# Kernel optimization log

Measured on AMD Instinct MI355X. Metric: run time of the kernel, lower is better.

Reference implementation:

```python
import jax, jax.numpy as jnp
import numpy as np

D = 1024
H = 16
HD = D // H
FF = 4 * D


def layer_norm(x, gamma, beta, eps=1e-5):
    mu = jnp.mean(x, axis=-1, keepdims=True)
    var = jnp.var(x, axis=-1, keepdims=True)
    return (x - mu) * jax.lax.rsqrt(var + eps) * gamma + beta


def setup_inputs() -> dict:
    key = jax.random.key(0)
    ks = jax.random.split(key, 12)
    B, Nq, Nkv = 8, 512, 1024
    s = 0.02
    return {
        "query": jax.random.normal(ks[0], (B, Nq, D), jnp.float32),
        "key_value": jax.random.normal(ks[1], (B, Nkv, D), jnp.float32),
        "key_padding_mask": jax.random.randint(ks[2], (B, Nkv), 0, 2) > 0,
        "nq_gamma": jnp.ones((D,), jnp.float32),
        "nq_beta": jnp.zeros((D,), jnp.float32),
        "nkv_gamma": jnp.ones((D,), jnp.float32),
        "nkv_beta": jnp.zeros((D,), jnp.float32),
        "in_proj_w": jax.random.normal(ks[3], (3 * D, D), jnp.float32) * s,
        "in_proj_b": jnp.zeros((3 * D,), jnp.float32),
        "out_w": jax.random.normal(ks[4], (D, D), jnp.float32) * s,
        "out_b": jnp.zeros((D,), jnp.float32),
        "nff_gamma": jnp.ones((D,), jnp.float32),
        "nff_beta": jnp.zeros((D,), jnp.float32),
        "ff1_w": jax.random.normal(ks[5], (FF, D), jnp.float32) * s,
        "ff1_b": jnp.zeros((FF,), jnp.float32),
        "ff2_w": jax.random.normal(ks[6], (D, FF), jnp.float32) * s,
        "ff2_b": jnp.zeros((D,), jnp.float32),
    }


def reference(query, key_value, key_padding_mask, nq_gamma, nq_beta, nkv_gamma,
              nkv_beta, in_proj_w, in_proj_b, out_w, out_b, nff_gamma, nff_beta,
              ff1_w, ff1_b, ff2_w, ff2_b):
    B, Nq, _ = query.shape
    Nkv = key_value.shape[1]

    q_in = layer_norm(query, nq_gamma, nq_beta)
    kv_in = layer_norm(key_value, nkv_gamma, nkv_beta)

    # packed in-projection as in torch MultiheadAttention
    wq, wk, wv = in_proj_w[:D], in_proj_w[D:2 * D], in_proj_w[2 * D:]
    bq, bk, bv = in_proj_b[:D], in_proj_b[D:2 * D], in_proj_b[2 * D:]
    q = (q_in @ wq.T + bq).reshape(B, Nq, H, HD).transpose(0, 2, 1, 3)   # b h q d
    k = (kv_in @ wk.T + bk).reshape(B, Nkv, H, HD).transpose(0, 2, 1, 3)  # b h k d
    v = (kv_in @ wv.T + bv).reshape(B, Nkv, H, HD).transpose(0, 2, 1, 3)

    scale = 1.0 / np.sqrt(HD).astype(np.float32)
    scores = jnp.einsum('bhqd,bhkd->bhqk', q, k) * scale
    neg = jnp.finfo(scores.dtype).min
    scores = jnp.where(key_padding_mask[:, None, None, :], neg, scores)
    attn = jax.nn.softmax(scores, axis=-1)                  # (B,H,Nq,Nkv)
    ctx = jnp.einsum('bhqk,bhkd->bhqd', attn, v)
    ctx = ctx.transpose(0, 2, 1, 3).reshape(B, Nq, D)
    attended = ctx @ out_w.T + out_b
    attn_weights = jnp.mean(attn, axis=1)                   # averaged over heads

    x = query + attended
    h = layer_norm(x, nff_gamma, nff_beta)
    h = jax.nn.gelu(h @ ff1_w.T + ff1_b, approximate=False)
    x = x + (h @ ff2_w.T + ff2_b)
    return (x, attn_weights)
```

## Files before the change

kernel.cpp:

```cpp
#include <hip/hip_runtime.h>
#include <hip/hip_bf16.h>
#include <math.h>

#define D    1024
#define NQ   512
#define NKV  1024
#define BATCH 8
#define NH   16
#define HD   64
#define FFD  4096

typedef short bf16x8 __attribute__((ext_vector_type(8)));
typedef float f32x4  __attribute__((ext_vector_type(4)));

static __device__ __forceinline__ float bf2f(__hip_bfloat16 x){ return __bfloat162float(x); }
static __device__ __forceinline__ unsigned short f2bbits(float f){
    __hip_bfloat16 h = __float2bfloat16(f);
    return *(unsigned short*)&h;
}

static __device__ __forceinline__ void gload_lds16(const __hip_bfloat16* g, __hip_bfloat16* l){
    __builtin_amdgcn_global_load_lds(
        (const __attribute__((address_space(1))) void*)g,
        (__attribute__((address_space(3))) void*)l,
        16, 0, 0);
}

__global__ __launch_bounds__(256) void cvt_w_kernel(const float* __restrict__ in,
                                                    __hip_bfloat16* __restrict__ out, int n)
{
    int i = blockIdx.x*256 + threadIdx.x;
    if (i < n) out[i] = __float2bfloat16(in[i]);
}

__global__ __launch_bounds__(256) void ln_kernel(
    const float* __restrict__ x, const float* __restrict__ gamma, const float* __restrict__ beta,
    __hip_bfloat16* __restrict__ out)
{
    int row = blockIdx.x, t = threadIdx.x;
    __shared__ float wsum[4];
    __shared__ float stat[2];
    float4 v = *(const float4*)&x[(size_t)row*D + t*4];
    float s = v.x+v.y+v.z+v.w;
    #pragma unroll
    for (int o=32;o>0;o>>=1) s += __shfl_down(s, o);
    if ((t&63)==0) wsum[t>>6] = s;
    __syncthreads();
    if (t==0) stat[0] = (wsum[0]+wsum[1]+wsum[2]+wsum[3])*(1.f/D);
    __syncthreads();
    float mu = stat[0];
    float d0=v.x-mu, d1=v.y-mu, d2=v.z-mu, d3=v.w-mu;
    float s2 = d0*d0+d1*d1+d2*d2+d3*d3;
    #pragma unroll
    for (int o=32;o>0;o>>=1) s2 += __shfl_down(s2, o);
    if ((t&63)==0) wsum[t>>6] = s2;
    __syncthreads();
    if (t==0) stat[1] = rsqrtf((wsum[0]+wsum[1]+wsum[2]+wsum[3])*(1.f/D) + 1e-5f);
    __syncthreads();
    float rs = stat[1];
    const float4 g = *(const float4*)&gamma[t*4];
    const float4 b = *(const float4*)&beta[t*4];
    union { unsigned short u[4]; short4 s4; } pk;
    pk.u[0]=f2bbits(d0*rs*g.x+b.x); pk.u[1]=f2bbits(d1*rs*g.y+b.y);
    pk.u[2]=f2bbits(d2*rs*g.z+b.z); pk.u[3]=f2bbits(d3*rs*g.w+b.w);
    *(short4*)&out[(size_t)row*D + t*4] = pk.s4;
}

#define BM 128
#define BN 128
#define BK 32

static __device__ __forceinline__ void stage128(
    const __hip_bfloat16* __restrict__ A, const __hip_bfloat16* __restrict__ W,
    int K, int bm, int bn, int k0,
    __hip_bfloat16* as, __hip_bfloat16* bs, int w, int srow, int scol)
{
    #pragma unroll
    for (int rep=0; rep<2; rep++){
        int ti = (w<<1) + rep;
        gload_lds16(&A[(size_t)(bm + ti*16 + srow)*K + k0 + scol], &as[ti*16*BK]);
        gload_lds16(&W[(size_t)(bn + ti*16 + srow)*K + k0 + scol], &bs[ti*16*BK]);
    }
}

static __device__ __forceinline__ void compute128(
    const __hip_bfloat16* as, const __hip_bfloat16* bs,
    int wm, int wn, int quad, int l16, f32x4 acc[4][4])
{
    bf16x8 af[4], bfr[4];
    #pragma unroll
    for (int i=0;i<4;i++) af[i]  = *(const bf16x8*)&as[(wm + 16*i + l16)*BK + quad*8];
    #pragma unroll
    for (int j=0;j<4;j++) bfr[j] = *(const bf16x8*)&bs[(wn + 16*j + l16)*BK + quad*8];
    #pragma unroll
    for (int i=0;i<4;i++)
        #pragma unroll
        for (int j=0;j<4;j++)
            acc[i][j] = __builtin_amdgcn_mfma_f32_16x16x32_bf16(af[i], bfr[j], acc[i][j], 0, 0, 0);
}

static __device__ __forceinline__ void gemm_loop(
    const __hip_bfloat16* __restrict__ A, const __hip_bfloat16* __restrict__ W,
    int K, int bm, int bn,
    __hip_bfloat16* As0, __hip_bfloat16* Bs0, __hip_bfloat16* As1, __hip_bfloat16* Bs1,
    f32x4 acc[4][4])
{
    const int t = threadIdx.x;
    const int w = t >> 6, lane = t & 63;
    const int quad = lane >> 4, l16 = lane & 15;
    const int wm = (w >> 1) * 64, wn = (w & 1) * 64;
    const int srow = lane >> 2, scol = (lane & 3) << 3;

    stage128(A, W, K, bm, bn, 0, As0, Bs0, w, srow, scol);
    __syncthreads();
    const int nt = K >> 5;
    for (int ts = 0; ts < nt; ts += 2){
        stage128(A, W, K, bm, bn, (ts+1)<<5, As1, Bs1, w, srow, scol);
        compute128(As0, Bs0, wm, wn, quad, l16, acc);
        __syncthreads();
        if (ts + 2 < nt)
            stage128(A, W, K, bm, bn, (ts+2)<<5, As0, Bs0, w, srow, scol);
        compute128(As1, Bs1, wm, wn, quad, l16, acc);
        __syncthreads();
    }
}

__global__ __launch_bounds__(256) void gemm_mfma_kernel(
    const __hip_bfloat16* __restrict__ A, const __hip_bfloat16* __restrict__ Wb,
    const float* __restrict__ bias, int biasOff,
    const float* __restrict__ residIn, const float* __restrict__ residF,
    float* __restrict__ Cf, __hip_bfloat16* __restrict__ Cb,
    int M, int N, int K, int gelu)
{
    __shared__ __hip_bfloat16 As0[BM*BK], Bs0[BN*BK], As1[BM*BK], Bs1[BN*BK];
    int bm = blockIdx.y * BM, bn = blockIdx.x * BN;
    f32x4 acc[4][4];
    #pragma unroll
    for (int i=0;i<4;i++)
        #pragma unroll
        for (int j=0;j<4;j++) acc[i][j] = (f32x4){0.f,0.f,0.f,0.f};

    gemm_loop(A, Wb, K, bm, bn, As0, Bs0, As1, Bs1, acc);

    const int t = threadIdx.x;
    const int w = t >> 6, lane = t & 63;
    const int quad = lane >> 4, l16 = lane & 15;
    const int wm = (w >> 1) * 64, wn = (w & 1) * 64;
    #pragma unroll
    for (int i=0;i<4;i++){
        #pragma unroll
        for (int j=0;j<4;j++){
            int colg = bn + wn + 16*j + l16;
            float bv = bias[biasOff + colg];
            #pragma unroll
            for (int r=0;r<4;r++){
                int rowg = bm + wm + 16*i + quad*4 + r;
                float vv = acc[i][j][r] + bv;
                if (gelu) vv = 0.5f*vv*(1.f + erff(vv*0.70710678118654752f));
                size_t idx = (size_t)rowg*N + colg;
                if (residIn) vv += residIn[idx];
                if (residF)  vv += residF[idx];
                if (Cf) Cf[idx] = vv;
                if (Cb) Cb[idx] = __float2bfloat16(vv);
            }
        }
    }
}

__global__ __launch_bounds__(256) void qkv_kernel(
    const __hip_bfloat16* __restrict__ qln, const __hip_bfloat16* __restrict__ kvln,
    const __hip_bfloat16* __restrict__ wip, const float* __restrict__ ipb,
    __hip_bfloat16* __restrict__ qb, __hip_bfloat16* __restrict__ kb,
    __hip_bfloat16* __restrict__ vbT)
{
    __shared__ __hip_bfloat16 As0[BM*BK], Bs0[BN*BK], As1[BM*BK], Bs1[BN*BK];
    int id = blockIdx.x;
    const __hip_bfloat16 *A, *W;
    int bm, bn, isq;
    if (id < 1024){ isq = 0; A = kvln; W = wip + (size_t)D*D; bn = (id & 15)*BN; bm = (id >> 4)*BM; }
    else { int qid = id - 1024; isq = 1; A = qln; W = wip; bn = (qid & 7)*BN; bm = (qid >> 3)*BM; }

    f32x4 acc[4][4];
    #pragma unroll
    for (int i=0;i<4;i++)
        #pragma unroll
        for (int j=0;j<4;j++) acc[i][j] = (f32x4){0.f,0.f,0.f,0.f};

    gemm_loop(A, W, 1024, bm, bn, As0, Bs0, As1, Bs1, acc);

    const int t = threadIdx.x;
    const int w = t >> 6, lane = t & 63;
    const int quad = lane >> 4, l16 = lane & 15;
    const int wm = (w >> 1) * 64, wn = (w & 1) * 64;
    #pragma unroll
    for (int i=0;i<4;i++){
        #pragma unroll
        for (int j=0;j<4;j++){
            int colg = bn + wn + 16*j + l16;
            float bv = ipb[(isq ? 0 : D) + colg];
            if (isq){
                #pragma unroll
                for (int r=0;r<4;r++){
                    int rowg = bm + wm + 16*i + quad*4 + r;
                    qb[(size_t)rowg*D + colg] = __float2bfloat16(acc[i][j][r] + bv);
                }
            } else if (colg < 1024){
                #pragma unroll
                for (int r=0;r<4;r++){
                    int rowg = bm + wm + 16*i + quad*4 + r;
                    kb[(size_t)rowg*D + colg] = __float2bfloat16(acc[i][j][r] + bv);
                }
            } else {
                union { unsigned short u[4]; short4 s4; } pk;
                #pragma unroll
                for (int r=0;r<4;r++) pk.u[r] = f2bbits(acc[i][j][r] + bv);
                int rowg0 = bm + wm + 16*i + quad*4;
                int bb = rowg0 >> 10, kvi = rowg0 & 1023;
                int c = colg - 1024, hh = c >> 6, dd = c & 63;
                *(short4*)&vbT[(((size_t)bb*NH + hh)*HD + dd)*NKV + kvi] = pk.s4;
            }
        }
    }
}

#define QT 16
#define PLD (NKV + 8)
__global__ __launch_bounds__(512) void attn_kernel(
    const __hip_bfloat16* __restrict__ q, const __hip_bfloat16* __restrict__ k,
    const __hip_bfloat16* __restrict__ vt, const void* __restrict__ mask,
    __hip_bfloat16* __restrict__ ctx, float* __restrict__ attn_out)
{
    const int t = threadIdx.x;
    const int w = t >> 6;
    const int lane = t & 63;
    const int g = lane >> 4;
    const int l16 = lane & 15;
    const int b  = blockIdx.x;
    const int q0 = blockIdx.y * QT;

    __shared__ __hip_bfloat16 P[QT*PLD];
    __shared__ float pvred[4*16*20];
    __shared__ float red[8*16];
    __shared__ int m8s;

    if (t==0) m8s = 0;
    __syncthreads();
    if (t < 256){ unsigned wd = ((const unsigned*)mask)[t]; if (wd > 1u) atomicOr(&m8s, 1); }
    __syncthreads();
    const bool m8 = m8s != 0;

    unsigned mbits = 0;
    #pragma unroll
    for (int kt=0;kt<8;kt++){
        #pragma unroll
        for (int r=0;r<4;r++){
            size_t mi = (size_t)b*NKV + w*128 + kt*16 + 4*g + r;
            int mv = m8 ? (int)((const unsigned char*)mask)[mi] : ((const int*)mask)[mi];
            if (mv) mbits |= (1u << (kt*4+r));
        }
    }

    float amean[8][4];
    #pragma unroll
    for (int kt=0;kt<8;kt++)
        #pragma unroll
        for (int r=0;r<4;r++) amean[kt][r] = 0.f;

    const int mt = w >> 1;
    const int kvh = w & 1;
    const __hip_bfloat16* qrow = &q[((size_t)(b*NQ + q0 + l16))*D];

    for (int h=0; h<NH; h++){
        bf16x8 bq0 = *(const bf16x8*)&qrow[h*HD + g*8];
        bf16x8 bq1 = *(const bf16x8*)&qrow[h*HD + 32 + g*8];
        f32x4 s[8];
        #pragma unroll
        for (int kt=0;kt<8;kt++){
            const __hip_bfloat16* kp = &k[((size_t)(b*NKV + w*128 + kt*16 + l16))*D + h*HD];
            bf16x8 a0 = *(const bf16x8*)&kp[g*8];
            bf16x8 a1 = *(const bf16x8*)&kp[32 + g*8];
            f32x4 z = (f32x4){0.f,0.f,0.f,0.f};
            z = __builtin_amdgcn_mfma_f32_16x16x32_bf16(a0, bq0, z, 0, 0, 0);
            z = __builtin_amdgcn_mfma_f32_16x16x32_bf16(a1, bq1, z, 0, 0, 0);
            s[kt] = z;
        }
        float lmax = -3.0e38f;
        #pragma unroll
        for (int kt=0;kt<8;kt++){
            #pragma unroll
            for (int r=0;r<4;r++){
                float sv = ((mbits >> (kt*4+r)) & 1u) ? -3.0e38f : s[kt][r]*0.125f;
                s[kt][r] = sv;
                lmax = fmaxf(lmax, sv);
            }
        }
        lmax = fmaxf(lmax, __shfl_xor(lmax, 16));
        lmax = fmaxf(lmax, __shfl_xor(lmax, 32));
        if (lane < 16) red[w*16 + l16] = lmax;
        __syncthreads();
        float m = red[l16];
        #pragma unroll
        for (int w2=1; w2<8; w2++) m = fmaxf(m, red[w2*16 + l16]);
        float lsum = 0.f;
        #pragma unroll
        for (int kt=0;kt<8;kt++){
            #pragma unroll
            for (int r=0;r<4;r++){
                float e = __expf(s[kt][r] - m);
                s[kt][r] = e;
                lsum += e;
            }
        }
        lsum += __shfl_xor(lsum, 16);
        lsum += __shfl_xor(lsum, 32);
        __syncthreads();
        if (lane < 16) red[w*16 + l16] = lsum;
        __syncthreads();
        float tot = red[l16];
        #pragma unroll
        for (int w2=1; w2<8; w2++) tot += red[w2*16 + l16];
        float inv = 1.f/tot;
        float ai  = inv * (1.f/NH);
        #pragma unroll
        for (int kt=0;kt<8;kt++){
            union { unsigned short u[4]; short4 s4; } pk;
            #pragma unroll
            for (int r=0;r<4;r++){
                amean[kt][r] += s[kt][r]*ai;
                pk.u[r] = f2bbits(s[kt][r]);
            }
            *(short4*)&P[l16*PLD + w*128 + kt*16 + 4*g] = pk.s4;
        }
        __syncthreads();
        f32x4 pv = (f32x4){0.f,0.f,0.f,0.f};
        const __hip_bfloat16* vrow = &vt[(((size_t)(b*NH + h))*HD + mt*16 + l16)*NKV + kvh*512];
        #pragma unroll
        for (int ks=0;ks<16;ks++){
            bf16x8 av = *(const bf16x8*)&vrow[ks*32 + g*8];
            bf16x8 bp = *(const bf16x8*)&P[l16*PLD + kvh*512 + ks*32 + g*8];
            pv = __builtin_amdgcn_mfma_f32_16x16x32_bf16(av, bp, pv, 0, 0, 0);
        }
        if (kvh){
            *(f32x4*)&pvred[(mt*16 + l16)*20 + 4*g] = pv;
        }
        __syncthreads();
        if (!kvh){
            const f32x4 other = *(const f32x4*)&pvred[(mt*16 + l16)*20 + 4*g];
            union { unsigned short u[4]; short4 s4; } pk;
            #pragma unroll
            for (int r=0;r<4;r++) pk.u[r] = f2bbits((pv[r] + other[r]) * inv);
            *(short4*)&ctx[((size_t)(b*NQ + q0 + l16))*D + h*HD + mt*16 + 4*g] = pk.s4;
        }
        __syncthreads();
    }
    float* ao = attn_out + ((size_t)(b*NQ + q0 + l16))*NKV;
    #pragma unroll
    for (int kt=0;kt<8;kt++){
        float4 v4 = make_float4(amean[kt][0], amean[kt][1], amean[kt][2], amean[kt][3]);
        *(float4*)&ao[w*128 + kt*16 + 4*g] = v4;
    }
}

__global__ __launch_bounds__(256) void fill_f32_kernel(float* __restrict__ p, float val, long n){
    size_t i = (size_t)blockIdx.x*256 + threadIdx.x;
    if ((long)i < n) p[i] = val;
}

extern "C" void kernel_launch(void* const* d_in, const int* in_sizes, int n_in,
                              void* d_out, int out_size, void* d_ws, size_t ws_size,
                              hipStream_t stream)
{
    const float* query     = (const float*)d_in[0];
    const float* key_value = (const float*)d_in[1];
    const void*  mask      = d_in[2];
    const float* nq_gamma  = (const float*)d_in[3];
    const float* nq_beta   = (const float*)d_in[4];
    const float* nkv_gamma = (const float*)d_in[5];
    const float* nkv_beta  = (const float*)d_in[6];
    const float* ipw       = (const float*)d_in[7];
    const float* ipb       = (const float*)d_in[8];
    const float* out_w     = (const float*)d_in[9];
    const float* out_b     = (const float*)d_in[10];
    const float* nffg      = (const float*)d_in[11];
    const float* nffb      = (const float*)d_in[12];
    const float* ff1w      = (const float*)d_in[13];
    const float* ff1b      = (const float*)d_in[14];
    const float* ff2w      = (const float*)d_in[15];
    const float* ff2b      = (const float*)d_in[16];

    float* out_x = (float*)d_out;
    long Dn  = (n_in > 3)  ? in_sizes[3]  : 0;
    long FFn = (n_in > 14) ? in_sizes[14] : 0;
    long Rq=0, Rkv=0, Nkvd=0, Bd=0, Nqd=0;
    auto derive = [&](long Sq_, long Skv_)->bool{
        if (Dn <= 0 || Sq_ <= 0 || Skv_ <= 0) return false;
        if (Sq_ % Dn || Skv_ % Dn) return false;
        Rq = Sq_/Dn; Rkv = Skv_/Dn;
        long num = (long)out_size - Rq*Dn;
        if (Rq <= 0 || num <= 0 || num % Rq) return false;
        Nkvd = num / Rq;
        if (Nkvd <= 0 || Rkv % Nkvd) return false;
        Bd = Rkv / Nkvd;
        if (Bd <= 0 || Rq % Bd) return false;
        Nqd = Rq / Bd;
        if ((long)in_sizes[2] != Rkv) return false;
        return true;
    };
    int sentinel = 0;
    if (n_in != 17) sentinel = 600;
    else if (!derive(in_sizes[0], in_sizes[1])) sentinel = 300;
    if (!sentinel && !(Dn==1024 && FFn==4096 && Bd==8 && Nqd==512 && Nkvd==1024)) sentinel = 500;
    if (!sentinel && ws_size < ((size_t)88<<20)) sentinel = 400;
    if (sentinel){
        long n = out_size;
        fill_f32_kernel<<<(unsigned)((n+255)/256), 256, 0, stream>>>(out_x, (float)sentinel, n);
        return;
    }

    float* out_attn = out_x + (size_t)BATCH*NQ*D;

    char* Wc = (char*)d_ws;
    __hip_bfloat16* wip  = (__hip_bfloat16*)(Wc);
    __hip_bfloat16* wout = (__hip_bfloat16*)(Wc + ((size_t)6<<20));
    __hip_bfloat16* wff1 = (__hip_bfloat16*)(Wc + ((size_t)8<<20));
    __hip_bfloat16* wff2 = (__hip_bfloat16*)(Wc + ((size_t)16<<20));
    __hip_bfloat16* qln  = (__hip_bfloat16*)(Wc + ((size_t)24<<20));
    __hip_bfloat16* kvln = (__hip_bfloat16*)(Wc + ((size_t)32<<20));
    __hip_bfloat16* qb   = (__hip_bfloat16*)(Wc + ((size_t)48<<20));
    __hip_bfloat16* kb   = (__hip_bfloat16*)(Wc + ((size_t)56<<20));
    __hip_bfloat16* vbT  = (__hip_bfloat16*)(Wc + ((size_t)72<<20));
    __hip_bfloat16* ctx  = (__hip_bfloat16*)(Wc + ((size_t)24<<20));
    float*          x1   = (float*)(Wc + ((size_t)32<<20));
    __hip_bfloat16* hln  = (__hip_bfloat16*)(Wc + ((size_t)48<<20));
    __hip_bfloat16* hge  = (__hip_bfloat16*)(Wc + ((size_t)56<<20));

    cvt_w_kernel<<<(3*1024*1024+255)/256, 256, 0, stream>>>(ipw,  wip,  3*1024*1024);
    cvt_w_kernel<<<(1024*1024+255)/256,   256, 0, stream>>>(out_w, wout, 1024*1024);
    cvt_w_kernel<<<(4*1024*1024+255)/256, 256, 0, stream>>>(ff1w, wff1, 4*1024*1024);
    cvt_w_kernel<<<(4*1024*1024+255)/256, 256, 0, stream>>>(ff2w, wff2, 4*1024*1024);
    ln_kernel<<<BATCH*NQ,  256, 0, stream>>>(query,     nq_gamma,  nq_beta,  qln);
    ln_kernel<<<BATCH*NKV, 256, 0, stream>>>(key_value, nkv_gamma, nkv_beta, kvln);
    qkv_kernel<<<1280, 256, 0, stream>>>(qln, kvln, wip, ipb, qb, kb, vbT);
    attn_kernel<<<dim3(BATCH, NQ/QT), 512, 0, stream>>>(qb, kb, vbT, mask, ctx, out_attn);
    gemm_mfma_kernel<<<dim3(8,32),  256, 0, stream>>>(ctx, wout, out_b, 0, query, nullptr, x1, nullptr, 4096, 1024, 1024, 0);
    ln_kernel<<<4096, 256, 0, stream>>>(x1, nffg, nffb, hln);
    gemm_mfma_kernel<<<dim3(32,32), 256, 0, stream>>>(hln, wff1, ff1b, 0, nullptr, nullptr, nullptr, hge, 4096, 4096, 1024, 1);
    gemm_mfma_kernel<<<dim3(8,32),  256, 0, stream>>>(hge, wff2, ff2b, 0, nullptr, x1, out_x, nullptr, 4096, 1024, 4096, 0);
}
```

Before: 607.9 us.

## Split attention heads across blocks and accumulate head-mean weights atomically

The attention kernel grid gains a third dimension that splits the 16 heads into 4 groups, so there are four times as many blocks to fill the GPU. Because each block now sees only part of the heads, the head-averaged attention weights are summed into the output with float atomicAdd, after a separate fill kernel zeroes that buffer. The per-head loop also drops two barriers: probabilities are written to shared memory inside the exp loop, and the max and sum reductions use separate shared buffers. In exchange it adds an extra full-size zeroing pass, many scalar atomics, and a summation order that is no longer deterministic.

```diff
diff --git a/kernel.cpp b/kernel.cpp
--- a/kernel.cpp
+++ b/kernel.cpp
@@ -224,6 +224,8 @@
 }
 
 #define QT 16
+#define HSPLIT 4
+#define HPB (NH/HSPLIT)
 #define PLD (NKV + 8)
 __global__ __launch_bounds__(512) void attn_kernel(
     const __hip_bfloat16* __restrict__ q, const __hip_bfloat16* __restrict__ k,
@@ -237,10 +239,12 @@
     const int l16 = lane & 15;
     const int b  = blockIdx.x;
     const int q0 = blockIdx.y * QT;
+    const int h0 = blockIdx.z * HPB;
 
     __shared__ __hip_bfloat16 P[QT*PLD];
     __shared__ float pvred[4*16*20];
-    __shared__ float red[8*16];
+    __shared__ float red1[8*16];
+    __shared__ float red2[8*16];
     __shared__ int m8s;
 
     if (t==0) m8s = 0;
@@ -270,7 +274,8 @@
     const int kvh = w & 1;
     const __hip_bfloat16* qrow = &q[((size_t)(b*NQ + q0 + l16))*D];
 
-    for (int h=0; h<NH; h++){
+    for (int hh=0; hh<HPB; hh++){
+        const int h = h0 + hh;
         bf16x8 bq0 = *(const bf16x8*)&qrow[h*HD + g*8];
         bf16x8 bq1 = *(const bf16x8*)&qrow[h*HD + 32 + g*8];
         f32x4 s[8];
@@ -296,42 +301,37 @@
         }
         lmax = fmaxf(lmax, __shfl_xor(lmax, 16));
         lmax = fmaxf(lmax, __shfl_xor(lmax, 32));
-        if (lane < 16) red[w*16 + l16] = lmax;
+        if (lane < 16) red1[w*16 + l16] = lmax;
         __syncthreads();
-        float m = red[l16];
-        #pragma unroll
-        for (int w2=1; w2<8; w2++) m = fmaxf(m, red[w2*16 + l16]);
+        float m = red1[l16];
+        #pragma unroll
+        for (int w2=1; w2<8; w2++) m = fmaxf(m, red1[w2*16 + l16]);
         float lsum = 0.f;
         #pragma unroll
         for (int kt=0;kt<8;kt++){
+            union { unsigned short u[4]; short4 s4; } pk;
             #pragma unroll
             for (int r=0;r<4;r++){
                 float e = __expf(s[kt][r] - m);
                 s[kt][r] = e;
                 lsum += e;
+                pk.u[r] = f2bbits(e);
             }
+            *(short4*)&P[l16*PLD + w*128 + kt*16 + 4*g] = pk.s4;
         }
         lsum += __shfl_xor(lsum, 16);
         lsum += __shfl_xor(lsum, 32);
+        if (lane < 16) red2[w*16 + l16] = lsum;
         __syncthreads();
-        if (lane < 16) red[w*16 + l16] = lsum;
-        __syncthreads();
-        float tot = red[l16];
-        #pragma unroll
-        for (int w2=1; w2<8; w2++) tot += red[w2*16 + l16];
+        float tot = red2[l16];
+        #pragma unroll
+        for (int w2=1; w2<8; w2++) tot += red2[w2*16 + l16];
         float inv = 1.f/tot;
         float ai  = inv * (1.f/NH);
         #pragma unroll
-        for (int kt=0;kt<8;kt++){
-            union { unsigned short u[4]; short4 s4; } pk;
+        for (int kt=0;kt<8;kt++)
             #pragma unroll
-            for (int r=0;r<4;r++){
-                amean[kt][r] += s[kt][r]*ai;
-                pk.u[r] = f2bbits(s[kt][r]);
-            }
-            *(short4*)&P[l16*PLD + w*128 + kt*16 + 4*g] = pk.s4;
-        }
-        __syncthreads();
+            for (int r=0;r<4;r++) amean[kt][r] += s[kt][r]*ai;
         f32x4 pv = (f32x4){0.f,0.f,0.f,0.f};
         const __hip_bfloat16* vrow = &vt[(((size_t)(b*NH + h))*HD + mt*16 + l16)*NKV + kvh*512];
         #pragma unroll
@@ -351,14 +351,13 @@
             for (int r=0;r<4;r++) pk.u[r] = f2bbits((pv[r] + other[r]) * inv);
             *(short4*)&ctx[((size_t)(b*NQ + q0 + l16))*D + h*HD + mt*16 + 4*g] = pk.s4;
         }
-        __syncthreads();
     }
     float* ao = attn_out + ((size_t)(b*NQ + q0 + l16))*NKV;
     #pragma unroll
-    for (int kt=0;kt<8;kt++){
-        float4 v4 = make_float4(amean[kt][0], amean[kt][1], amean[kt][2], amean[kt][3]);
-        *(float4*)&ao[w*128 + kt*16 + 4*g] = v4;
-    }
+    for (int kt=0;kt<8;kt++)
+        #pragma unroll
+        for (int r=0;r<4;r++)
+            atomicAdd(&ao[w*128 + kt*16 + 4*g + r], amean[kt][r]);
 }
 
 __global__ __launch_bounds__(256) void fill_f32_kernel(float* __restrict__ p, float val, long n){
@@ -441,7 +440,8 @@
     ln_kernel<<<BATCH*NQ,  256, 0, stream>>>(query,     nq_gamma,  nq_beta,  qln);
     ln_kernel<<<BATCH*NKV, 256, 0, stream>>>(key_value, nkv_gamma, nkv_beta, kvln);
     qkv_kernel<<<1280, 256, 0, stream>>>(qln, kvln, wip, ipb, qb, kb, vbT);
-    attn_kernel<<<dim3(BATCH, NQ/QT), 512, 0, stream>>>(qb, kb, vbT, mask, ctx, out_attn);
+    fill_f32_kernel<<<(unsigned)(((long)BATCH*NQ*NKV+255)/256), 256, 0, stream>>>(out_attn, 0.f, (long)BATCH*NQ*NKV);
+    attn_kernel<<<dim3(BATCH, NQ/QT, HSPLIT), 512, 0, stream>>>(qb, kb, vbT, mask, ctx, out_attn);
     gemm_mfma_kernel<<<dim3(8,32),  256, 0, stream>>>(ctx, wout, out_b, 0, query, nullptr, x1, nullptr, 4096, 1024, 1024, 0);
     ln_kernel<<<4096, 256, 0, stream>>>(x1, nffg, nffb, hln);
     gemm_mfma_kernel<<<dim3(32,32), 256, 0, stream>>>(hln, wff1, ff1b, 0, nullptr, nullptr, nullptr, hge, 4096, 4096, 1024, 1);
```

Result: slower. 770.6 us (+26.8%).
